# Performance work log

Hardware: AMD Instinct MI355X
Metric: run time of the kernel (lower is better)

## Reference

```python
import jax, jax.numpy as jnp
import numpy as np

N, G, L, C = 32768, 128, 256, 128   # nodes, graphs, nodes-per-graph, channels
E, DS, DC, DR = 524288, 16, 4, 8    # edges, d_state, d_conv, dt_rank
EPS = 1e-5


def setup_inputs():
    key = jax.random.key(0)
    ks = jax.random.split(key, 16)
    s = 0.02
    p = lambda i, shape: jax.random.normal(ks[i], shape, jnp.float32) * s
    return {
        "x": jax.random.normal(ks[0], (N, C), jnp.float32),
        "edge_index": jax.random.randint(ks[1], (2, E), 0, N),
        "batch": jnp.repeat(jnp.arange(G), L),  # uniform graph sizes, sorted
        "gin_eps": jnp.float32(0.0),
        "gin_w1": p(2, (C, C)), "gin_b1": jnp.zeros((C,), jnp.float32),
        "gin_w2": p(3, (C, C)), "gin_b2": jnp.zeros((C,), jnp.float32),
        "in_proj_w": p(4, (2 * C, C)),
        "conv_w": p(5, (C, DC)), "conv_b": jnp.zeros((C,), jnp.float32),
        "x_proj_w": p(6, (DR + 2 * DS, C)),
        "dt_proj_w": p(7, (C, DR)),
        "dt_proj_b": jnp.full((C,), -4.0, jnp.float32),  # softplus -> small dt
        "A_log": jnp.log(jnp.broadcast_to(jnp.arange(1, DS + 1, dtype=jnp.float32), (C, DS))),
        "Dp": jnp.ones((C,), jnp.float32),
        "out_proj_w": p(8, (C, C)),
        "mlp_w1": p(9, (2 * C, C)), "mlp_b1": jnp.zeros((2 * C,), jnp.float32),
        "mlp_w2": p(10, (C, 2 * C)), "mlp_b2": jnp.zeros((C,), jnp.float32),
        "g1": jnp.ones((C,), jnp.float32), "be1": jnp.zeros((C,), jnp.float32),
        "g2": jnp.ones((C,), jnp.float32), "be2": jnp.zeros((C,), jnp.float32),
        "g3": jnp.ones((C,), jnp.float32), "be3": jnp.zeros((C,), jnp.float32),
    }


def batch_norm(h, g, b):
    # BatchNorm1d forward (batch statistics, biased var), eps=1e-5
    mu = h.mean(0)
    var = h.var(0)
    return (h - mu) * jax.lax.rsqrt(var + EPS) * g + b


def mamba(xd, in_proj_w, conv_w, conv_b, x_proj_w, dt_proj_w, dt_proj_b, A_log, Dp, out_proj_w):
    # xd: [G, L, C]; Mamba with expand=1 (d_inner == C)
    xz = jnp.einsum('glc,dc->gld', xd, in_proj_w)        # [G,L,2C]
    xs, z = jnp.split(xz, 2, axis=-1)
    # depthwise causal conv1d, kernel DC, left-pad DC-1
    xc = jax.lax.conv_general_dilated(
        xs.transpose(0, 2, 1), conv_w[:, None, :], (1,), [(DC - 1, 0)],
        dimension_numbers=('NCH', 'OIH', 'NCH'), feature_group_count=C)
    xs = jax.nn.silu(xc.transpose(0, 2, 1) + conv_b)     # [G,L,C]
    xdbl = jnp.einsum('gld,ed->gle', xs, x_proj_w)       # [G,L,DR+2*DS]
    dtr, Bm, Cm = jnp.split(xdbl, [DR, DR + DS], axis=-1)
    dt = jax.nn.softplus(jnp.einsum('glr,dr->gld', dtr, dt_proj_w) + dt_proj_b)  # [G,L,C]
    A = -jnp.exp(A_log)                                   # [C,DS]

    def step(hst, t):
        dt_t, B_t, C_t, x_t = t                           # [G,C],[G,DS],[G,DS],[G,C]
        dA = jnp.exp(dt_t[..., None] * A)                 # [G,C,DS]
        hst = dA * hst + dt_t[..., None] * B_t[:, None, :] * x_t[..., None]
        return hst, (hst * C_t[:, None, :]).sum(-1)       # y_t: [G,C]

    h0 = jnp.zeros((G, C, DS), xd.dtype)
    _, y = jax.lax.scan(step, h0, (dt.transpose(1, 0, 2), Bm.transpose(1, 0, 2),
                                   Cm.transpose(1, 0, 2), xs.transpose(1, 0, 2)))
    y = y.transpose(1, 0, 2) + Dp * xs                    # [G,L,C]
    y = y * jax.nn.silu(z)
    return jnp.einsum('gld,cd->glc', y, out_proj_w)


def _forward(edge_index, x, gin_eps, gin_w1, gin_b1, gin_w2, gin_b2,
             in_proj_w, conv_w, conv_b, x_proj_w, dt_proj_w, dt_proj_b,
             A_log, Dp, out_proj_w, mlp_w1, mlp_b1, mlp_w2, mlp_b2,
             g1, be1, g2, be2, g3, be3):
    # --- local MPNN branch: GIN conv + residual + norm1 (dropout=0, eval) ---
    agg = jax.ops.segment_sum(x[edge_index[0]], edge_index[1], num_segments=N)
    hg = (1.0 + gin_eps) * x + agg
    hg = jax.nn.relu(hg @ gin_w1.T + gin_b1) @ gin_w2.T + gin_b2
    h1 = batch_norm(hg + x, g1, be1)
    # --- Mamba branch over dense batch (uniform sizes -> reshape, mask all-true) ---
    xd = x.reshape(G, L, C)
    hm = mamba(xd, in_proj_w, conv_w, conv_b, x_proj_w, dt_proj_w, dt_proj_b,
               A_log, Dp, out_proj_w).reshape(N, C)
    h2 = batch_norm(hm + x, g2, be2)
    # --- combine + MLP + norm3 ---
    out = h1 + h2
    out = out + (jax.nn.relu(out @ mlp_w1.T + mlp_b1) @ mlp_w2.T + mlp_b2)
    out = batch_norm(out, g3, be3)
    return out, h2


def reference(x, edge_index, batch, gin_eps, gin_w1, gin_b1, gin_w2, gin_b2,
              in_proj_w, conv_w, conv_b, x_proj_w, dt_proj_w, dt_proj_b,
              A_log, Dp, out_proj_w, mlp_w1, mlp_b1, mlp_w2, mlp_b2,
              g1, be1, g2, be2, g3, be3):
    del batch  # uniform graph sizes encoded in (G, L)
    return _forward(edge_index, x, gin_eps, gin_w1, gin_b1, gin_w2, gin_b2,
                    in_proj_w, conv_w, conv_b, x_proj_w, dt_proj_w, dt_proj_b,
                    A_log, Dp, out_proj_w, mlp_w1, mlp_b1, mlp_w2, mlp_b2,
                    g1, be1, g2, be2, g3, be3)
```

## Files before the change

kernel.cpp:

```cpp
#include <hip/hip_runtime.h>
#include <hip/hip_bf16.h>

#define NN 32768
#define GG 128
#define LL 256
#define CC 128
#define EE 524288
#define NCHUNK 8
#define TCH 32

typedef __attribute__((ext_vector_type(8))) short short8v;
typedef __attribute__((ext_vector_type(4))) short short4v;
typedef __attribute__((ext_vector_type(4))) float floatx4;

__device__ inline short f2bf(float f) {
    __hip_bfloat16 h = __float2bfloat16(f);
    short s; __builtin_memcpy(&s, &h, 2); return s;
}
__device__ inline float b2f(unsigned short u) {
    unsigned v = ((unsigned)u) << 16; float f; __builtin_memcpy(&f, &v, 4); return f;
}
__device__ inline floatx4 mfma16(short8v a, short8v b, floatx4 c) {
    return __builtin_amdgcn_mfma_f32_16x16x32_bf16(a, b, c, 0, 0, 0);
}
__device__ inline float softplus_f(float v) {
    return (v > 20.f) ? v : __logf(1.f + __expf(v));
}

__global__ __launch_bounds__(256)
void prep_kernel(const float* __restrict__ x,
                 const float* __restrict__ gw1, const float* __restrict__ gw2,
                 const float* __restrict__ ipw, const float* __restrict__ xpw,
                 const float* __restrict__ opw, const float* __restrict__ mw1,
                 const float* __restrict__ mw2, const float* __restrict__ dtw,
                 unsigned short* __restrict__ wb, int* __restrict__ cnt,
                 float* __restrict__ stats, unsigned short* __restrict__ xb)
{
    int b = blockIdx.x, tid = threadIdx.x;
    if (b < 74) {
        const float* src; int dstoff, lb;
        if (b < 8)       { src = gw1;        dstoff = 0;      lb = b; }
        else if (b < 16) { src = gw2;        dstoff = 16384;  lb = b - 8; }
        else if (b < 32) { src = ipw;        dstoff = 32768;  lb = b - 16; }
        else if (b < 34) { src = xpw + 1024; dstoff = 81920;  lb = b - 32; }
        else if (b < 42) { src = opw;        dstoff = 86016;  lb = b - 34; }
        else if (b < 58) { src = mw1;        dstoff = 102400; lb = b - 42; }
        else             { src = mw2;        dstoff = 135168; lb = b - 58; }
        size_t i = (size_t)lb * 2048 + tid * 8;
        float4 a = *(const float4*)(src + i);
        float4 c = *(const float4*)(src + i + 4);
        short8v s = { f2bf(a.x), f2bf(a.y), f2bf(a.z), f2bf(a.w),
                      f2bf(c.x), f2bf(c.y), f2bf(c.z), f2bf(c.w) };
        *(short8v*)(wb + dstoff + i) = s;
    } else if (b < 138) {
        int i = (b - 74) * 256 + tid;
        int d = i >> 7, c = i & 127;
        float s = 0.f;
#pragma unroll
        for (int r = 0; r < 8; r++) s = fmaf(dtw[d * 8 + r], xpw[r * 128 + c], s);
        wb[65536 + i] = (unsigned short)f2bf(s);
    } else if (b < 170) {
        int idx = (b - 138) * 1024 + tid * 4;
        *(int4*)(cnt + idx) = make_int4(0, 0, 0, 0);
    } else if (b == 170) {
        stats[tid] = 0.f; stats[256 + tid] = 0.f; stats[512 + tid] = 0.f;
    } else {
        size_t i = (size_t)(b - 171) * 256 + tid;
        float4 a = *(const float4*)(x + i * 8);
        float4 c = *(const float4*)(x + i * 8 + 4);
        short8v s = { f2bf(a.x), f2bf(a.y), f2bf(a.z), f2bf(a.w),
                      f2bf(c.x), f2bf(c.y), f2bf(c.z), f2bf(c.w) };
        *(short8v*)(xb + i * 8) = s;
    }
}

__global__ __launch_bounds__(256)
void front_hist_kernel(const unsigned short* __restrict__ xb,
                 const unsigned short* __restrict__ ipwb,
                 const float* __restrict__ cw, const float* __restrict__ cb,
                 const unsigned short* __restrict__ wdtb, const float* __restrict__ dtbv,
                 const unsigned short* __restrict__ xpwb,
                 const float* __restrict__ Alog,
                 unsigned short* __restrict__ xsb, unsigned short* __restrict__ zb,
                 unsigned short* __restrict__ dtout, float* __restrict__ BCout,
                 float* __restrict__ Q, float* __restrict__ SDT,
                 const int* __restrict__ ei, int* __restrict__ cnt)
{
    __shared__ __align__(16) unsigned char smem[48 * 136 * 2 + 32 * 136 * 2 + TCH * 16 * 4];
    const int tid = threadIdx.x;
    if (blockIdx.x >= 1024) {
        int e = (blockIdx.x - 1024) * 256 + tid;
        atomicAdd(&cnt[ei[EE + e]], 1);
        return;
    }
    unsigned short* xsL = (unsigned short*)smem;
    unsigned short* xcL = xsL + 48 * 136;
    float* BsL = (float*)(xcL + 32 * 136);
    const int lane = tid & 63;
    const int wv = tid >> 6;
    const int rql = lane & 15;
    const int kseg = (lane >> 4) * 8;
    const int rsub = (lane >> 4) * 4;
    const int fb = blockIdx.x;
    const int R0 = fb * 32;
    const int RB = R0 - 16;
    const int g = fb >> 3;
    const int chunk = fb & 7;

    int coln[4];
#pragma unroll
    for (int n = 0; n < 4; n++) coln[n] = wv * 64 + n * 16 + rql;
    short8v wr[4][4];
#pragma unroll
    for (int n = 0; n < 4; n++) {
        const unsigned short* wp = ipwb + (size_t)coln[n] * 128 + kseg;
#pragma unroll
        for (int kk = 0; kk < 4; kk++) wr[n][kk] = *(const short8v*)(wp + kk * 32);
    }
    int arow[3];
#pragma unroll
    for (int m = 0; m < 3; m++) {
        int r = RB + m * 16 + rql;
        arow[m] = r < 0 ? 0 : r;
    }
    floatx4 acc[3][4];
#pragma unroll
    for (int m = 0; m < 3; m++)
#pragma unroll
        for (int n = 0; n < 4; n++)
#pragma unroll
            for (int r = 0; r < 4; r++) acc[m][n][r] = 0.f;
#pragma unroll
    for (int kb = 0; kb < 4; kb += 2) {
        short8v a2[3][2];
#pragma unroll
        for (int m = 0; m < 3; m++)
#pragma unroll
            for (int j = 0; j < 2; j++)
                a2[m][j] = *(const short8v*)(xb + (size_t)arow[m] * 128 + kseg + (kb + j) * 32);
        __builtin_amdgcn_sched_barrier(0);
#pragma unroll
        for (int j = 0; j < 2; j++)
#pragma unroll
            for (int m = 0; m < 3; m++)
#pragma unroll
                for (int n = 0; n < 4; n++)
                    acc[m][n] = mfma16(a2[m][j], wr[n][kb + j], acc[m][n]);
    }
    if (wv < 2) {
#pragma unroll
        for (int m = 0; m < 3; m++)
#pragma unroll
            for (int r = 0; r < 4; r++) {
                int row_l = m * 16 + rsub + r;
#pragma unroll
                for (int n = 0; n < 4; n++)
                    xsL[row_l * 136 + coln[n]] = (unsigned short)f2bf(acc[m][n][r]);
            }
    } else {
#pragma unroll
        for (int m = 1; m < 3; m++)
#pragma unroll
            for (int r = 0; r < 4; r++) {
                int row_g = RB + m * 16 + rsub + r;
#pragma unroll
                for (int n = 0; n < 4; n++)
                    zb[(size_t)row_g * 128 + (coln[n] - 128)] = (unsigned short)f2bf(acc[m][n][r]);
            }
    }
    __syncthreads();

    {
        int r = tid >> 3;
        int c0 = (tid & 7) * 16;
        int l = (R0 + r) & (LL - 1);
        const unsigned short* basep = &xsL[(16 + r) * 136 + c0];
        unsigned short o16[16];
#pragma unroll
        for (int half = 0; half < 2; half++) {
            short8v x0 = *(const short8v*)(basep + half * 8);
            short8v x1 = *(const short8v*)(basep - 136 + half * 8);
            short8v x2 = *(const short8v*)(basep - 272 + half * 8);
            short8v x3 = *(const short8v*)(basep - 408 + half * 8);
#pragma unroll
            for (int j = 0; j < 8; j++) {
                int c = c0 + half * 8 + j;
                float4 w = *(const float4*)(cw + c * 4);
                float v = cb[c];
                v = fmaf(b2f((unsigned short)x0[j]), w.w, v);
                if (l >= 1) v = fmaf(b2f((unsigned short)x1[j]), w.z, v);
                if (l >= 2) v = fmaf(b2f((unsigned short)x2[j]), w.y, v);
                if (l >= 3) v = fmaf(b2f((unsigned short)x3[j]), w.x, v);
                v = v / (1.f + __expf(-v));
                o16[half * 8 + j] = (unsigned short)f2bf(v);
            }
        }
#pragma unroll
        for (int half = 0; half < 2; half++) {
            short8v s;
#pragma unroll
            for (int j = 0; j < 8; j++) s[j] = (short)o16[half * 8 + j];
            *(short8v*)&xcL[r * 136 + c0 + half * 8] = s;
            *(short8v*)(xsb + (size_t)(R0 + r) * 128 + c0 + half * 8) = s;
        }
    }
    __syncthreads();

    unsigned short* dtL = xsL;
    int cold0 = wv * 32 + rql, cold1 = cold0 + 16;
    short8v wd0[4], wd1[4];
    {
        const unsigned short* wp0 = wdtb + (size_t)cold0 * 128 + kseg;
        const unsigned short* wp1 = wdtb + (size_t)cold1 * 128 + kseg;
#pragma unroll
        for (int kk = 0; kk < 4; kk++) {
            wd0[kk] = *(const short8v*)(wp0 + kk * 32);
            wd1[kk] = *(const short8v*)(wp1 + kk * 32);
        }
    }
    float bd0 = dtbv[cold0], bd1 = dtbv[cold1];
    int colb = wv * 16 + rql;
    short8v wbc[4];
    if (wv < 2) {
        const unsigned short* wp = xpwb + (size_t)colb * 128 + kseg;
#pragma unroll
        for (int kk = 0; kk < 4; kk++) wbc[kk] = *(const short8v*)(wp + kk * 32);
    }
    short8v a0[4], a1[4];
#pragma unroll
    for (int kk = 0; kk < 4; kk++) {
        a0[kk] = *(const short8v*)&xcL[rql * 136 + kseg + kk * 32];
        a1[kk] = *(const short8v*)&xcL[(16 + rql) * 136 + kseg + kk * 32];
    }
    floatx4 accd[2][2], accb[2];
#pragma unroll
    for (int m = 0; m < 2; m++) {
#pragma unroll
        for (int n = 0; n < 2; n++)
#pragma unroll
            for (int r = 0; r < 4; r++) accd[m][n][r] = 0.f;
#pragma unroll
        for (int r = 0; r < 4; r++) accb[m][r] = 0.f;
    }
#pragma unroll
    for (int kk = 0; kk < 4; kk++) {
        accd[0][0] = mfma16(a0[kk], wd0[kk], accd[0][0]);
        accd[0][1] = mfma16(a0[kk], wd1[kk], accd[0][1]);
        accd[1][0] = mfma16(a1[kk], wd0[kk], accd[1][0]);
        accd[1][1] = mfma16(a1[kk], wd1[kk], accd[1][1]);
        if (wv < 2) {
            accb[0] = mfma16(a0[kk], wbc[kk], accb[0]);
            accb[1] = mfma16(a1[kk], wbc[kk], accb[1]);
        }
    }
#pragma unroll
    for (int m = 0; m < 2; m++) {
#pragma unroll
        for (int r = 0; r < 4; r++) {
            int tl = m * 16 + rsub + r;
            int row_g = R0 + tl;
            float v0 = softplus_f(accd[m][0][r] + bd0);
            float v1 = softplus_f(accd[m][1][r] + bd1);
            unsigned short u0 = (unsigned short)f2bf(v0);
            unsigned short u1 = (unsigned short)f2bf(v1);
            dtout[(size_t)row_g * 128 + cold0] = u0;
            dtout[(size_t)row_g * 128 + cold1] = u1;
            dtL[tl * 136 + cold0] = u0;
            dtL[tl * 136 + cold1] = u1;
            if (wv < 2) {
                BCout[(size_t)row_g * 32 + colb] = accb[m][r];
                if (wv == 0) BsL[tl * 16 + colb] = accb[m][r];
            }
        }
    }
    __syncthreads();

    for (int u = tid; u < 512; u += 256) {
        int c = u >> 2, sp = u & 3;
        float ae0 = -__expf(Alog[c * 16 + sp * 4 + 0]);
        float ae1 = -__expf(Alog[c * 16 + sp * 4 + 1]);
        float ae2 = -__expf(Alog[c * 16 + sp * 4 + 2]);
        float ae3 = -__expf(Alog[c * 16 + sp * 4 + 3]);
        float q0 = 0, q1 = 0, q2 = 0, q3 = 0, sdt = 0;
        for (int t = TCH - 1; t >= 0; --t) {
            float dtv = b2f(dtL[t * 136 + c]);
            float xv  = b2f(xcL[t * 136 + c]);
            float uu = dtv * xv;
            const float* bs = &BsL[t * 16 + sp * 4];
            q0 = fmaf(__expf(ae0 * sdt) * uu, bs[0], q0);
            q1 = fmaf(__expf(ae1 * sdt) * uu, bs[1], q1);
            q2 = fmaf(__expf(ae2 * sdt) * uu, bs[2], q2);
            q3 = fmaf(__expf(ae3 * sdt) * uu, bs[3], q3);
            sdt += dtv;
        }
        float4* qp = (float4*)(Q + (((size_t)g * NCHUNK + chunk) * CC + c) * 16 + sp * 4);
        *qp = make_float4(q0, q1, q2, q3);
        if (sp == 0) SDT[((size_t)g * NCHUNK + chunk) * CC + c] = sdt;
    }
}

__global__ __launch_bounds__(1024)
void scanB_kernel(const int* __restrict__ cnt, int* __restrict__ base,
                  int* __restrict__ cursor,
                  const float* __restrict__ Q, const float* __restrict__ SDT,
                  const float* __restrict__ Alog, float* __restrict__ Hin)
{
    int tid = threadIdx.x;
    if (blockIdx.x == 0) {
        __shared__ int part[1024];
        int local[32];
        int s = 0;
#pragma unroll
        for (int j = 0; j < 32; j++) { local[j] = cnt[tid * 32 + j]; s += local[j]; }
        part[tid] = s;
        __syncthreads();
        for (int off = 1; off < 1024; off <<= 1) {
            int v = (tid >= off) ? part[tid - off] : 0;
            __syncthreads();
            part[tid] += v;
            __syncthreads();
        }
        int run = part[tid] - s;
#pragma unroll
        for (int j = 0; j < 32; j++) {
            base[tid * 32 + j] = run;
            cursor[tid * 32 + j] = run;
            run += local[j];
        }
        if (tid == 0) base[NN] = EE;
        return;
    }
    int idx = (blockIdx.x - 1) * 1024 + tid;
    int g = idx >> 11;
    int cs = idx & 2047;
    float ae = -__expf(Alog[cs]);
    float h = 0.f;
#pragma unroll
    for (int k = 0; k < NCHUNK; k++) {
        size_t o = ((size_t)g * NCHUNK + k);
        Hin[o * 2048 + cs] = h;
        float sdt = SDT[o * CC + (cs >> 4)];
        h = fmaf(__expf(ae * sdt), h, Q[o * 2048 + cs]);
    }
}

__global__ __launch_bounds__(256) void permute_kernel(const int* __restrict__ ei,
    int* __restrict__ cursor, int* __restrict__ perm)
{
    int e = blockIdx.x * 256 + threadIdx.x;
    int dst = ei[EE + e];
    int pos = atomicAdd(&cursor[dst], 1);
    perm[pos] = ei[e];
}

__global__ __launch_bounds__(512)
void scanout_gather_kernel(const float* __restrict__ BCp,
    const unsigned short* __restrict__ dtp, const unsigned short* __restrict__ xsp_,
    const unsigned short* __restrict__ zb, const float* __restrict__ Alog,
    const float* __restrict__ Dp, const float* __restrict__ Hin,
    const unsigned short* __restrict__ opwb, const unsigned short* __restrict__ xb,
    float* __restrict__ p2, float* ssum, float* ssq,
    const int* __restrict__ perm, const int* __restrict__ base,
    const float* __restrict__ epsp, unsigned short* __restrict__ hgin)
{
    __shared__ __align__(16) unsigned char smem[31232];
    const int tid = threadIdx.x;
    if (blockIdx.x >= 1024) {
        int node = (blockIdx.x - 1024) * 16 + (tid >> 5);
        int c4 = tid & 31;
        int b0 = base[node], b1 = base[node + 1];
        float s0 = 0, s1 = 0, s2 = 0, s3 = 0;
        float t0 = 0, t1 = 0, t2 = 0, t3 = 0;
        int i = b0;
        for (; i + 1 < b1; i += 2) {
            short4v v0 = *(const short4v*)(xb + (size_t)perm[i] * CC + c4 * 4);
            short4v v1 = *(const short4v*)(xb + (size_t)perm[i + 1] * CC + c4 * 4);
            s0 += b2f((unsigned short)v0[0]); s1 += b2f((unsigned short)v0[1]);
            s2 += b2f((unsigned short)v0[2]); s3 += b2f((unsigned short)v0[3]);
            t0 += b2f((unsigned short)v1[0]); t1 += b2f((unsigned short)v1[1]);
            t2 += b2f((unsigned short)v1[2]); t3 += b2f((unsigned short)v1[3]);
        }
        if (i < b1) {
            short4v v0 = *(const short4v*)(xb + (size_t)perm[i] * CC + c4 * 4);
            s0 += b2f((unsigned short)v0[0]); s1 += b2f((unsigned short)v0[1]);
            s2 += b2f((unsigned short)v0[2]); s3 += b2f((unsigned short)v0[3]);
        }
        float e1 = 1.f + epsp[0];
        short4v xv = *(const short4v*)(xb + (size_t)node * CC + c4 * 4);
        float r0 = fmaf(e1, b2f((unsigned short)xv[0]), s0 + t0);
        float r1 = fmaf(e1, b2f((unsigned short)xv[1]), s1 + t1);
        float r2 = fmaf(e1, b2f((unsigned short)xv[2]), s2 + t2);
        float r3 = fmaf(e1, b2f((unsigned short)xv[3]), s3 + t3);
        short4v o = { f2bf(r0), f2bf(r1), f2bf(r2), f2bf(r3) };
        *(short4v*)(hgin + (size_t)node * CC + c4 * 4) = o;
        return;
    }
    float* BCs = (float*)smem;
    unsigned short* dts = (unsigned short*)(smem + 4096);
    unsigned short* xss = (unsigned short*)(smem + 12800);
    unsigned short* yL  = (unsigned short*)(smem + 21504);
    float* sred = (float*)(smem + 30208);
    const int b = blockIdx.x;
    const int g = b >> 3, chunk = b & 7;
    const int t0 = chunk * TCH;
    if (tid < 256) sred[tid] = 0.f;
    for (int i4 = tid; i4 < TCH * 8; i4 += 512) {
        int t = i4 >> 3, j4 = i4 & 7;
        *(float4*)&BCs[t * 32 + j4 * 4] =
            *(const float4*)(BCp + (size_t)(g * LL + t0 + t) * 32 + j4 * 4);
    }
    {
        int t = tid >> 4, c8 = tid & 15;
        size_t off = (size_t)(g * LL + t0 + t) * CC + c8 * 8;
        *(short8v*)&dts[t * 136 + c8 * 8] = *(const short8v*)(dtp + off);
        *(short8v*)&xss[t * 136 + c8 * 8] = *(const short8v*)(xsp_ + off);
    }
    const int c = tid >> 2, sp = tid & 3;
    float ae0 = -__expf(Alog[c * 16 + sp * 4 + 0]);
    float ae1 = -__expf(Alog[c * 16 + sp * 4 + 1]);
    float ae2 = -__expf(Alog[c * 16 + sp * 4 + 2]);
    float ae3 = -__expf(Alog[c * 16 + sp * 4 + 3]);
    float dpc = Dp[c];
    float4 hv = *(const float4*)(Hin + ((size_t)g * NCHUNK + chunk) * 2048 + c * 16 + sp * 4);
    float h0 = hv.x, h1 = hv.y, h2 = hv.z, h3 = hv.w;
    __syncthreads();
    const unsigned short* zg = zb + (size_t)(g * LL + t0) * CC + c;
    for (int t = 0; t < TCH; t++) {
        float dtv = b2f(dts[t * 136 + c]);
        float xv  = b2f(xss[t * 136 + c]);
        float u = dtv * xv;
        const float* bc = &BCs[t * 32 + sp * 4];
        h0 = fmaf(__expf(dtv * ae0), h0, u * bc[0]);
        h1 = fmaf(__expf(dtv * ae1), h1, u * bc[1]);
        h2 = fmaf(__expf(dtv * ae2), h2, u * bc[2]);
        h3 = fmaf(__expf(dtv * ae3), h3, u * bc[3]);
        float y = h0 * bc[16] + h1 * bc[17] + h2 * bc[18] + h3 * bc[19];
        y += __shfl_xor(y, 1);
        y += __shfl_xor(y, 2);
        if (sp == 0) {
            float zv = b2f(zg[t * CC]);
            float yo = fmaf(dpc, xv, y);
            yL[t * 136 + c] = (unsigned short)f2bf(yo * (zv / (1.f + __expf(-zv))));
        }
    }
    __syncthreads();

    const int lane = tid & 63;
    const int wv = tid >> 6;
    const int rql = lane & 15;
    const int kseg = (lane >> 4) * 8;
    const int rsub = (lane >> 4) * 4;
    const int colg = wv * 16 + rql;
    short8v w[4];
    {
        const unsigned short* wp = opwb + (size_t)colg * 128 + kseg;
#pragma unroll
        for (int kk = 0; kk < 4; kk++) w[kk] = *(const short8v*)(wp + kk * 32);
    }
    floatx4 acc[2];
#pragma unroll
    for (int m = 0; m < 2; m++)
#pragma unroll
        for (int r = 0; r < 4; r++) acc[m][r] = 0.f;
#pragma unroll
    for (int kk = 0; kk < 4; kk++) {
        short8v alo = *(const short8v*)&yL[rql * 136 + kseg + kk * 32];
        short8v ahi = *(const short8v*)&yL[(16 + rql) * 136 + kseg + kk * 32];
        acc[0] = mfma16(alo, w[kk], acc[0]);
        acc[1] = mfma16(ahi, w[kk], acc[1]);
    }
    float sumr = 0.f, sqr = 0.f;
#pragma unroll
    for (int m = 0; m < 2; m++) {
#pragma unroll
        for (int r = 0; r < 4; r++) {
            int row_g = g * LL + t0 + m * 16 + rsub + r;
            float v = acc[m][r] + b2f(xb[(size_t)row_g * CC + colg]);
            p2[(size_t)row_g * CC + colg] = v;
            sumr += v; sqr += v * v;
        }
    }
    sumr += __shfl_xor(sumr, 16); sumr += __shfl_xor(sumr, 32);
    sqr  += __shfl_xor(sqr, 16);  sqr  += __shfl_xor(sqr, 32);
    if ((lane >> 4) == 0) {
        atomicAdd(&sred[colg], sumr);
        atomicAdd(&sred[128 + colg], sqr);
    }
    __syncthreads();
    if (tid < 128) {
        atomicAdd(&ssum[tid], sred[tid]);
        atomicAdd(&ssq[tid], sred[128 + tid]);
    }
}

template<int KMID>
__global__ __launch_bounds__(256)
void fused2(const unsigned short* __restrict__ A,
            const unsigned short* __restrict__ W1b, const float* __restrict__ b1,
            const unsigned short* __restrict__ W2b, const float* __restrict__ b2,
            const unsigned short* __restrict__ residb,
            float* __restrict__ outp,
            float* ssum, float* ssq)
{
    constexpr int NF1 = KMID / 64;
    constexpr int NK1 = 4;
    constexpr int NK2 = KMID / 32;
    constexpr int LDSW = KMID + 8;
    __shared__ unsigned short lds[2][32 * LDSW];
    __shared__ float sred[256];
    const int tid = threadIdx.x;
    const int lane = tid & 63;
    const int wc = tid >> 6;
    const int rql = lane & 15;
    const int kseg = (lane >> 4) * 8;
    const int rsub = (lane >> 4) * 4;

    sred[tid] = 0.f;

    short8v w1r[NF1][NK1];
    int colg1[NF1];
    float b1c[NF1];
#pragma unroll
    for (int f = 0; f < NF1; f++) {
        colg1[f] = wc * (16 * NF1) + f * 16 + rql;
        const unsigned short* wp = W1b + (size_t)colg1[f] * 128 + kseg;
#pragma unroll
        for (int kk = 0; kk < NK1; kk++) w1r[f][kk] = *(const short8v*)(wp + kk * 32);
        b1c[f] = b1[colg1[f]];
    }
    int colg2[2];
    colg2[0] = wc * 32 + rql;
    colg2[1] = colg2[0] + 16;
    float b2c[2] = { b2[colg2[0]], b2[colg2[1]] };
    float ssumr[2] = {0.f, 0.f}, ssqr[2] = {0.f, 0.f};

    short8v abuf[2][NK1][2];
    {
        const unsigned short* ap = A + (size_t)(blockIdx.x * 32 + rql) * 128 + kseg;
#pragma unroll
        for (int kk = 0; kk < NK1; kk++) {
            abuf[0][kk][0] = *(const short8v*)(ap + kk * 32);
            abuf[0][kk][1] = *(const short8v*)(ap + 16 * 128 + kk * 32);
        }
    }
    __syncthreads();

#pragma unroll
    for (int t = 0; t < 2; t++) {
        const int R0 = (blockIdx.x + t * 512) * 32;
        floatx4 acc1[2][NF1];
#pragma unroll
        for (int m = 0; m < 2; m++)
#pragma unroll
            for (int f = 0; f < NF1; f++)
#pragma unroll
                for (int r = 0; r < 4; r++) acc1[m][f][r] = 0.f;
#pragma unroll
        for (int kk = 0; kk < NK1; kk++)
#pragma unroll
            for (int m = 0; m < 2; m++)
#pragma unroll
                for (int f = 0; f < NF1; f++)
                    acc1[m][f] = mfma16(abuf[t][kk][m], w1r[f][kk], acc1[m][f]);
        unsigned short* L = &lds[t][0];
#pragma unroll
        for (int m = 0; m < 2; m++)
#pragma unroll
            for (int f = 0; f < NF1; f++)
#pragma unroll
                for (int r = 0; r < 4; r++) {
                    float v = fmaxf(acc1[m][f][r] + b1c[f], 0.f);
                    L[(m * 16 + rsub + r) * LDSW + colg1[f]] = (unsigned short)f2bf(v);
                }
        __syncthreads();
        if (t == 0) {
            const unsigned short* ap = A + (size_t)((blockIdx.x + 512) * 32 + rql) * 128 + kseg;
#pragma unroll
            for (int kk = 0; kk < NK1; kk++) {
                abuf[1][kk][0] = *(const short8v*)(ap + kk * 32);
                abuf[1][kk][1] = *(const short8v*)(ap + 16 * 128 + kk * 32);
            }
        }
        short8v w2a[NK2], w2b[NK2];
        {
            const unsigned short* wq0 = W2b + (size_t)colg2[0] * KMID + kseg;
            const unsigned short* wq1 = W2b + (size_t)colg2[1] * KMID + kseg;
#pragma unroll
            for (int kk = 0; kk < NK2; kk++) {
                w2a[kk] = *(const short8v*)(wq0 + kk * 32);
                w2b[kk] = *(const short8v*)(wq1 + kk * 32);
            }
        }
        floatx4 acc2[2][2];
#pragma unroll
        for (int m = 0; m < 2; m++)
#pragma unroll
            for (int n = 0; n < 2; n++)
#pragma unroll
                for (int r = 0; r < 4; r++) acc2[m][n][r] = 0.f;
#pragma unroll
        for (int kk = 0; kk < NK2; kk++) {
            short8v a2lo = *(const short8v*)&L[rql * LDSW + kseg + kk * 32];
            short8v a2hi = *(const short8v*)&L[(rql + 16) * LDSW + kseg + kk * 32];
            acc2[0][0] = mfma16(a2lo, w2a[kk], acc2[0][0]);
            acc2[0][1] = mfma16(a2lo, w2b[kk], acc2[0][1]);
            acc2[1][0] = mfma16(a2hi, w2a[kk], acc2[1][0]);
            acc2[1][1] = mfma16(a2hi, w2b[kk], acc2[1][1]);
        }
#pragma unroll
        for (int m = 0; m < 2; m++) {
#pragma unroll
            for (int r = 0; r < 4; r++) {
                int row_g = R0 + m * 16 + rsub + r;
#pragma unroll
                for (int n = 0; n < 2; n++) {
                    float v = acc2[m][n][r] + b2c[n];
                    v += b2f(residb[(size_t)row_g * CC + colg2[n]]);
                    outp[(size_t)row_g * CC + colg2[n]] = v;
                    ssumr[n] += v; ssqr[n] += v * v;
                }
            }
        }
    }
    __syncthreads();
#pragma unroll
    for (int n = 0; n < 2; n++) {
        atomicAdd(&sred[colg2[n]], ssumr[n]);
        atomicAdd(&sred[128 + colg2[n]], ssqr[n]);
    }
    __syncthreads();
    if (tid < 128) {
        atomicAdd(&ssum[tid], sred[tid]);
        atomicAdd(&ssq[tid], sred[128 + tid]);
    }
}

__global__ __launch_bounds__(256) void norm12_kernel(const float* __restrict__ p1,
    const float* __restrict__ p2, const float* __restrict__ stats,
    const float* g1, const float* be1, const float* g2, const float* be2,
    float* __restrict__ h2out, unsigned short* __restrict__ out12b)
{
    __shared__ float sc[512];
    int tid = threadIdx.x;
    if (tid < 128) {
        int c = tid;
        const float inv = 1.0f / NN;
        float m1 = stats[c] * inv;
        float v1 = fmaxf(stats[128 + c] * inv - m1 * m1, 0.f);
        float i1 = rsqrtf(v1 + 1e-5f);
        sc[c] = g1[c] * i1; sc[128 + c] = be1[c] - m1 * g1[c] * i1;
        float m2 = stats[256 + c] * inv;
        float v2 = fmaxf(stats[384 + c] * inv - m2 * m2, 0.f);
        float i2 = rsqrtf(v2 + 1e-5f);
        sc[256 + c] = g2[c] * i2; sc[384 + c] = be2[c] - m2 * g2[c] * i2;
    }
    __syncthreads();
    size_t idx = (size_t)blockIdx.x * 256 + tid;
    int c4 = (int)(idx & 31);
    float4 s1 = *(float4*)&sc[c4 * 4];
    float4 t1 = *(float4*)&sc[128 + c4 * 4];
    float4 s2 = *(float4*)&sc[256 + c4 * 4];
    float4 t2 = *(float4*)&sc[384 + c4 * 4];
    float4 a = *(const float4*)(p1 + idx * 4);
    float4 b = *(const float4*)(p2 + idx * 4);
    float4 h, o;
    h.x = fmaf(b.x, s2.x, t2.x); o.x = fmaf(a.x, s1.x, t1.x) + h.x;
    h.y = fmaf(b.y, s2.y, t2.y); o.y = fmaf(a.y, s1.y, t1.y) + h.y;
    h.z = fmaf(b.z, s2.z, t2.z); o.z = fmaf(a.z, s1.z, t1.z) + h.z;
    h.w = fmaf(b.w, s2.w, t2.w); o.w = fmaf(a.w, s1.w, t1.w) + h.w;
    *(float4*)(h2out + idx * 4) = h;
    short4v ob = { f2bf(o.x), f2bf(o.y), f2bf(o.z), f2bf(o.w) };
    *(short4v*)(out12b + idx * 4) = ob;
}

__global__ __launch_bounds__(256) void norm3_kernel(const float* __restrict__ p3,
    const float* __restrict__ stats, const float* g3, const float* be3,
    float* __restrict__ outp)
{
    __shared__ float sc[256];
    int tid = threadIdx.x;
    if (tid < 128) {
        int c = tid;
        const float inv = 1.0f / NN;
        float m = stats[512 + c] * inv;
        float v = fmaxf(stats[640 + c] * inv - m * m, 0.f);
        float iv = rsqrtf(v + 1e-5f);
        sc[c] = g3[c] * iv; sc[128 + c] = be3[c] - m * g3[c] * iv;
    }
    __syncthreads();
    size_t idx = (size_t)blockIdx.x * 256 + tid;
    int c4 = (int)(idx & 31);
    float4 s = *(float4*)&sc[c4 * 4];
    float4 t = *(float4*)&sc[128 + c4 * 4];
    float4 a = *(const float4*)(p3 + idx * 4);
    float4 o;
    o.x = fmaf(a.x, s.x, t.x); o.y = fmaf(a.y, s.y, t.y);
    o.z = fmaf(a.z, s.z, t.z); o.w = fmaf(a.w, s.w, t.w);
    *(float4*)(outp + idx * 4) = o;
}

extern "C" void kernel_launch(void* const* d_in, const int* in_sizes, int n_in,
                              void* d_out, int out_size, void* d_ws, size_t ws_size,
                              hipStream_t stream)
{
    (void)in_sizes; (void)n_in; (void)out_size; (void)ws_size;
    const float* x    = (const float*)d_in[0];
    const int*   ei   = (const int*)d_in[1];
    const float* eps  = (const float*)d_in[3];
    const float* gw1  = (const float*)d_in[4];
    const float* gb1  = (const float*)d_in[5];
    const float* gw2  = (const float*)d_in[6];
    const float* gb2  = (const float*)d_in[7];
    const float* ipw  = (const float*)d_in[8];
    const float* cw   = (const float*)d_in[9];
    const float* cb   = (const float*)d_in[10];
    const float* xpw  = (const float*)d_in[11];
    const float* dtw  = (const float*)d_in[12];
    const float* dtb  = (const float*)d_in[13];
    const float* Alog = (const float*)d_in[14];
    const float* Dp   = (const float*)d_in[15];
    const float* opw  = (const float*)d_in[16];
    const float* mw1  = (const float*)d_in[17];
    const float* mb1  = (const float*)d_in[18];
    const float* mw2  = (const float*)d_in[19];
    const float* mb2  = (const float*)d_in[20];
    const float* g1   = (const float*)d_in[21];
    const float* be1  = (const float*)d_in[22];
    const float* g2   = (const float*)d_in[23];
    const float* be2  = (const float*)d_in[24];
    const float* g3   = (const float*)d_in[25];
    const float* be3  = (const float*)d_in[26];

    float* outp = (float*)d_out;
    float* h2o  = outp + (size_t)NN * CC;
    float* p1 = outp;
    float* p2 = h2o;

    const size_t M1 = 1u << 20;
    float* ws = (float*)d_ws;
    float*  scr4   = ws;
    float*  BC     = ws + 4 * M1;
    unsigned short* zb      = (unsigned short*)(ws + 7 * M1);
    unsigned short* dtb_buf = (unsigned short*)(ws + 9 * M1);
    unsigned short* xb      = (unsigned short*)(ws + 11 * M1);
    unsigned short* hgin    = (unsigned short*)(ws + 13 * M1);
    unsigned short* xsb     = (unsigned short*)(ws + 15 * M1);
    unsigned short* out12b  = (unsigned short*)(ws + 17 * M1);
    float*  stats  = ws + 19 * M1;
    int*    cnt    = (int*)(stats + 768);
    int*    baseA  = cnt + NN;
    int*    cursor = baseA + NN + 1;
    int*    perm   = cursor + NN;
    float*  SDT    = (float*)(perm + EE);
    unsigned short* wbase = (unsigned short*)(SDT + 131072);
    unsigned short* gw1b = wbase;
    unsigned short* gw2b = wbase + 16384;
    unsigned short* ipwb = wbase + 32768;
    unsigned short* wdtb = wbase + 65536;
    unsigned short* xpwb = wbase + 81920;
    unsigned short* opwb = wbase + 86016;
    unsigned short* mw1b = wbase + 102400;
    unsigned short* mw2b = wbase + 135168;

    float* Qbuf = scr4;
    float* Hin  = scr4 + 2 * M1;
    float* p3   = scr4;

    prep_kernel<<<dim3(171 + 2048), 256, 0, stream>>>(
        x, gw1, gw2, ipw, xpw, opw, mw1, mw2, dtw, wbase, cnt, stats, xb);

    front_hist_kernel<<<dim3(3072), 256, 0, stream>>>(
        xb, ipwb, cw, cb, wdtb, dtb, xpwb, Alog, xsb, zb, dtb_buf, BC, Qbuf, SDT,
        ei, cnt);

    scanB_kernel<<<dim3(257), 1024, 0, stream>>>(cnt, baseA, cursor, Qbuf, SDT, Alog, Hin);

    permute_kernel<<<dim3(EE / 256), 256, 0, stream>>>(ei, cursor, perm);

    scanout_gather_kernel<<<dim3(3072), 512, 0, stream>>>(
        BC, dtb_buf, xsb, zb, Alog, Dp, Hin, opwb, xb, p2, stats + 256, stats + 384,
        perm, baseA, eps, hgin);

    fused2<128><<<dim3(512), 256, 0, stream>>>(
        hgin, gw1b, gb1, gw2b, gb2, xb, p1, stats + 0, stats + 128);

    norm12_kernel<<<dim3(NN * CC / 4 / 256), 256, 0, stream>>>(
        p1, p2, stats, g1, be1, g2, be2, h2o, out12b);

    fused2<256><<<dim3(512), 256, 0, stream>>>(
        out12b, mw1b, mb1, mw2b, mb2, out12b, p3, stats + 512, stats + 640);

    norm3_kernel<<<dim3(NN * CC / 4 / 256), 256, 0, stream>>>(p3, stats, g3, be3, outp);
}
```

Baseline: 248.7 us.

## Reschedule CSR build stages across kernels to remove a launch

Moves the destination histogram into the prep kernel and the exclusive scan into an extra block of the front Mamba kernel. The edge permutation now runs in the same launch as the chunk-state combine, so one launch is removed and each index-building step overlaps with heavier Mamba work. Zeroing of the counters and stats buffers switches to hipMemsetAsync. The scan now runs in a single 256-thread block that reads the counts twice, which could become a tail on the front kernel.

```diff
diff --git a/kernel.cpp b/kernel.cpp
--- a/kernel.cpp
+++ b/kernel.cpp
@@ -33,8 +33,8 @@
                  const float* __restrict__ ipw, const float* __restrict__ xpw,
                  const float* __restrict__ opw, const float* __restrict__ mw1,
                  const float* __restrict__ mw2, const float* __restrict__ dtw,
-                 unsigned short* __restrict__ wb, int* __restrict__ cnt,
-                 float* __restrict__ stats, unsigned short* __restrict__ xb)
+                 unsigned short* __restrict__ wb, unsigned short* __restrict__ xb,
+                 const int* __restrict__ ei, int* __restrict__ cnt)
 {
     int b = blockIdx.x, tid = threadIdx.x;
     if (b < 74) {
@@ -59,23 +59,21 @@
 #pragma unroll
         for (int r = 0; r < 8; r++) s = fmaf(dtw[d * 8 + r], xpw[r * 128 + c], s);
         wb[65536 + i] = (unsigned short)f2bf(s);
-    } else if (b < 170) {
-        int idx = (b - 138) * 1024 + tid * 4;
-        *(int4*)(cnt + idx) = make_int4(0, 0, 0, 0);
-    } else if (b == 170) {
-        stats[tid] = 0.f; stats[256 + tid] = 0.f; stats[512 + tid] = 0.f;
-    } else {
-        size_t i = (size_t)(b - 171) * 256 + tid;
+    } else if (b < 2186) {
+        size_t i = (size_t)(b - 138) * 256 + tid;
         float4 a = *(const float4*)(x + i * 8);
         float4 c = *(const float4*)(x + i * 8 + 4);
         short8v s = { f2bf(a.x), f2bf(a.y), f2bf(a.z), f2bf(a.w),
                       f2bf(c.x), f2bf(c.y), f2bf(c.z), f2bf(c.w) };
         *(short8v*)(xb + i * 8) = s;
+    } else {
+        int e = (b - 2186) * 256 + tid;
+        atomicAdd(&cnt[ei[EE + e]], 1);
     }
 }
 
 __global__ __launch_bounds__(256)
-void front_hist_kernel(const unsigned short* __restrict__ xb,
+void frontB_kernel(const unsigned short* __restrict__ xb,
                  const unsigned short* __restrict__ ipwb,
                  const float* __restrict__ cw, const float* __restrict__ cb,
                  const unsigned short* __restrict__ wdtb, const float* __restrict__ dtbv,
@@ -84,13 +82,31 @@
                  unsigned short* __restrict__ xsb, unsigned short* __restrict__ zb,
                  unsigned short* __restrict__ dtout, float* __restrict__ BCout,
                  float* __restrict__ Q, float* __restrict__ SDT,
-                 const int* __restrict__ ei, int* __restrict__ cnt)
+                 const int* __restrict__ cnt, int* __restrict__ base,
+                 int* __restrict__ cursor)
 {
     __shared__ __align__(16) unsigned char smem[48 * 136 * 2 + 32 * 136 * 2 + TCH * 16 * 4];
     const int tid = threadIdx.x;
-    if (blockIdx.x >= 1024) {
-        int e = (blockIdx.x - 1024) * 256 + tid;
-        atomicAdd(&cnt[ei[EE + e]], 1);
+    if (blockIdx.x == 1024) {
+        __shared__ int part[256];
+        int s = 0;
+        for (int j = 0; j < 128; j++) s += cnt[tid * 128 + j];
+        part[tid] = s;
+        __syncthreads();
+        for (int off = 1; off < 256; off <<= 1) {
+            int v = (tid >= off) ? part[tid - off] : 0;
+            __syncthreads();
+            part[tid] += v;
+            __syncthreads();
+        }
+        int run = part[tid] - s;
+        for (int j = 0; j < 128; j++) {
+            int v = cnt[tid * 128 + j];
+            base[tid * 128 + j] = run;
+            cursor[tid * 128 + j] = run;
+            run += v;
+        }
+        if (tid == 0) base[NN] = EE;
         return;
     }
     unsigned short* xsL = (unsigned short*)smem;
@@ -299,38 +315,21 @@
     }
 }
 
-__global__ __launch_bounds__(1024)
-void scanB_kernel(const int* __restrict__ cnt, int* __restrict__ base,
-                  int* __restrict__ cursor,
-                  const float* __restrict__ Q, const float* __restrict__ SDT,
-                  const float* __restrict__ Alog, float* __restrict__ Hin)
+__global__ __launch_bounds__(256)
+void combC_kernel(const float* __restrict__ Q, const float* __restrict__ SDT,
+                  const float* __restrict__ Alog, float* __restrict__ Hin,
+                  const int* __restrict__ ei, int* __restrict__ cursor,
+                  int* __restrict__ perm)
 {
     int tid = threadIdx.x;
-    if (blockIdx.x == 0) {
-        __shared__ int part[1024];
-        int local[32];
-        int s = 0;
-#pragma unroll
-        for (int j = 0; j < 32; j++) { local[j] = cnt[tid * 32 + j]; s += local[j]; }
-        part[tid] = s;
-        __syncthreads();
-        for (int off = 1; off < 1024; off <<= 1) {
-            int v = (tid >= off) ? part[tid - off] : 0;
-            __syncthreads();
-            part[tid] += v;
-            __syncthreads();
-        }
-        int run = part[tid] - s;
-#pragma unroll
-        for (int j = 0; j < 32; j++) {
-            base[tid * 32 + j] = run;
-            cursor[tid * 32 + j] = run;
-            run += local[j];
-        }
-        if (tid == 0) base[NN] = EE;
+    if (blockIdx.x >= 1024) {
+        int e = (blockIdx.x - 1024) * 256 + tid;
+        int dst = ei[EE + e];
+        int pos = atomicAdd(&cursor[dst], 1);
+        perm[pos] = ei[e];
         return;
     }
-    int idx = (blockIdx.x - 1) * 1024 + tid;
+    int idx = blockIdx.x * 256 + tid;
     int g = idx >> 11;
     int cs = idx & 2047;
     float ae = -__expf(Alog[cs]);
@@ -342,15 +341,6 @@
         float sdt = SDT[o * CC + (cs >> 4)];
         h = fmaf(__expf(ae * sdt), h, Q[o * 2048 + cs]);
     }
-}
-
-__global__ __launch_bounds__(256) void permute_kernel(const int* __restrict__ ei,
-    int* __restrict__ cursor, int* __restrict__ perm)
-{
-    int e = blockIdx.x * 256 + threadIdx.x;
-    int dst = ei[EE + e];
-    int pos = atomicAdd(&cursor[dst], 1);
-    perm[pos] = ei[e];
 }
 
 __global__ __launch_bounds__(512)
@@ -766,16 +756,17 @@
     float* Hin  = scr4 + 2 * M1;
     float* p3   = scr4;
 
-    prep_kernel<<<dim3(171 + 2048), 256, 0, stream>>>(
-        x, gw1, gw2, ipw, xpw, opw, mw1, mw2, dtw, wbase, cnt, stats, xb);
-
-    front_hist_kernel<<<dim3(3072), 256, 0, stream>>>(
+    hipMemsetAsync(cnt, 0, NN * sizeof(int), stream);
+    hipMemsetAsync(stats, 0, 768 * sizeof(float), stream);
+
+    prep_kernel<<<dim3(4234), 256, 0, stream>>>(
+        x, gw1, gw2, ipw, xpw, opw, mw1, mw2, dtw, wbase, xb, ei, cnt);
+
+    frontB_kernel<<<dim3(1025), 256, 0, stream>>>(
         xb, ipwb, cw, cb, wdtb, dtb, xpwb, Alog, xsb, zb, dtb_buf, BC, Qbuf, SDT,
-        ei, cnt);
-
-    scanB_kernel<<<dim3(257), 1024, 0, stream>>>(cnt, baseA, cursor, Qbuf, SDT, Alog, Hin);
-
-    permute_kernel<<<dim3(EE / 256), 256, 0, stream>>>(ei, cursor, perm);
+        cnt, baseA, cursor);
+
+    combC_kernel<<<dim3(3072), 256, 0, stream>>>(Qbuf, SDT, Alog, Hin, ei, cursor, perm);
 
     scanout_gather_kernel<<<dim3(3072), 512, 0, stream>>>(
         BC, dtb_buf, xsb, zb, Alog, Dp, Hin, opwb, xb, p2, stats + 256, stats + 384,
```

Measured after the change: 263.2 us. +5.8%, slower.
